# Kernel tuning notes

Hardware: AMD Instinct MI355X
Metric: run time of the kernel (lower is better)

## Reference

```python
import jax, jax.numpy as jnp
import numpy as np

NEG_SLOPE = 0.2  # LeakyReLU slope from the module


def setup_inputs() -> dict:
    key = jax.random.key(0)
    k1, k2, k3, k4 = jax.random.split(key, 4)
    B, N, C, H, D = 8, 1024, 256, 4, 64
    x = jax.random.normal(k1, (B, N, C), dtype=jnp.float32)
    adj = (jax.random.uniform(k2, (B, N, N)) < 0.05).astype(jnp.float32)
    # nn.Linear weight, stored as (in, out) for x @ W
    W = jax.random.normal(k3, (C, H * D), dtype=jnp.float32) / np.sqrt(C)
    a = jax.random.normal(k4, (1, H, 2 * D), dtype=jnp.float32) * 0.1
    return {"x": x, "adj": adj, "W": W, "a": a}


def reference(x, adj, W, a):
    # x: (B,N,C), adj: (B,N,N), W: (C,H*D), a: (1,H,2D)
    B, N, _ = x.shape
    H = a.shape[1]
    D = a.shape[2] // 2
    Wx = (x @ W).reshape(B, N, H, D)  # (B,N,H,D)
    # (cat([Wx_i, Wx_j]) * a).sum(-1) decomposes into two rank-1 terms:
    a_i, a_j = a[0, :, :D], a[0, :, D:]
    e_i = jnp.einsum('bnhd,hd->bnh', Wx, a_i)  # contribution of target node i
    e_j = jnp.einsum('bjhd,hd->bjh', Wx, a_j)  # contribution of source node j
    e = e_i[:, :, None, :] + e_j[:, None, :, :]  # (B,N,N,H)
    e = jnp.where(e > 0, e, NEG_SLOPE * e)  # LeakyReLU(0.2)
    # add self-loops, mask non-edges with -inf
    adj_self = adj + jnp.eye(N, dtype=adj.dtype)[None]
    mask = (adj_self == 0)[..., None]  # (B,N,N,1)
    e = jnp.where(mask, -jnp.inf, e)
    alpha = jax.nn.softmax(e, axis=2)  # softmax over neighbors j
    # dropout is identity in eval mode
    # torch: einsum('bnjh,bnjhd', alpha, Wx_j) with Wx_j broadcast over n
    out = jnp.einsum('bnjh,bjhd->bnhd', alpha, Wx)
    return out.reshape(B, N, H * D)
```

## Files before the change

### kernel.cpp

```cpp
#include <hip/hip_runtime.h>

#define Nn 1024
#define Cc 256
#define Hh 4
#define Dd 64
#define HD 256
#define LOG2E 1.4426950408889634f

typedef unsigned short u16;
typedef unsigned int u32;
typedef unsigned long long u64;
typedef unsigned char u8;
typedef __bf16 bf16x8 __attribute__((ext_vector_type(8)));
typedef float f32x4 __attribute__((ext_vector_type(4)));
typedef u16 u16x8 __attribute__((ext_vector_type(8)));
typedef u32 u32x4 __attribute__((ext_vector_type(4)));

__device__ __forceinline__ float bf2f(u16 v) {
    return __builtin_bit_cast(float, (u32)v << 16);
}
__device__ __forceinline__ u16 f2bf(float f) {
    u32 u = __builtin_bit_cast(u32, f);
    return (u16)((u + 0x7fffu + ((u >> 16) & 1u)) >> 16);
}
__device__ __forceinline__ float fast_exp2(float x) {
#if __has_builtin(__builtin_amdgcn_exp2f)
    return __builtin_amdgcn_exp2f(x);
#else
    float r; asm("v_exp_f32 %0, %1" : "=v"(r) : "v"(x)); return r;
#endif
}

__global__ __launch_bounds__(256) void k_bitmask_prep(const float* __restrict__ adj,
        u8* __restrict__ bm, const float* __restrict__ W,
        u16* __restrict__ WTh, u16* __restrict__ WTl) {
    int idx = blockIdx.x * 256 + threadIdx.x;
    int bn = idx >> 7;
    int byteidx = idx & 127;
    int n = bn & 1023;
    const float* p = adj + ((size_t)bn << 10) + (byteidx << 3);
    float4 v0 = *reinterpret_cast<const float4*>(p);
    float4 v1 = *reinterpret_cast<const float4*>(p + 4);
    u32 bits = 0;
    bits |= (__builtin_bit_cast(u32, v0.x) != 0u) ? 1u : 0u;
    bits |= (__builtin_bit_cast(u32, v0.y) != 0u) ? 2u : 0u;
    bits |= (__builtin_bit_cast(u32, v0.z) != 0u) ? 4u : 0u;
    bits |= (__builtin_bit_cast(u32, v0.w) != 0u) ? 8u : 0u;
    bits |= (__builtin_bit_cast(u32, v1.x) != 0u) ? 16u : 0u;
    bits |= (__builtin_bit_cast(u32, v1.y) != 0u) ? 32u : 0u;
    bits |= (__builtin_bit_cast(u32, v1.z) != 0u) ? 64u : 0u;
    bits |= (__builtin_bit_cast(u32, v1.w) != 0u) ? 128u : 0u;
    if ((n >> 3) == byteidx) bits |= 1u << (n & 7);
    bm[idx] = (u8)bits;
    if (blockIdx.x < 256) {
        int c = blockIdx.x;
        int t = threadIdx.x;
        float v = W[c * HD + t];
        u16 hi = f2bf(v);
        float lo = v - bf2f(hi);
        WTh[t * Cc + c] = hi;
        WTl[t * Cc + c] = f2bf(lo);
    }
}

__global__ __launch_bounds__(256) void k_gemm_xw(const float* __restrict__ x,
        const u16* __restrict__ WTh, const u16* __restrict__ WTl,
        const float* __restrict__ a, u16* __restrict__ WxTt,
        float* __restrict__ ei, float* __restrict__ ej) {
    int wave = blockIdx.x * 4 + (threadIdx.x >> 6);
    int lane = threadIdx.x & 63;
    int row_tile = wave >> 2;
    int h = wave & 3;
    int m0 = row_tile * 16;
    int b = m0 >> 10;
    int nloc0 = m0 & 1023;
    int c15 = lane & 15;
    int quad = lane >> 4;

    f32x4 acc[4] = {};
    const float* xrow = x + (size_t)(m0 + c15) * Cc + quad * 8;
    #pragma unroll
    for (int k0 = 0; k0 < Cc; k0 += 32) {
        float4 xv0 = *reinterpret_cast<const float4*>(xrow + k0);
        float4 xv1 = *reinterpret_cast<const float4*>(xrow + k0 + 4);
        float xv[8] = {xv0.x, xv0.y, xv0.z, xv0.w, xv1.x, xv1.y, xv1.z, xv1.w};
        u16x8 xh, xl;
        #pragma unroll
        for (int i = 0; i < 8; ++i) {
            u16 hb = f2bf(xv[i]);
            xh[i] = hb;
            xl[i] = f2bf(xv[i] - bf2f(hb));
        }
        bf16x8 ah = __builtin_bit_cast(bf16x8, xh);
        bf16x8 al = __builtin_bit_cast(bf16x8, xl);
        #pragma unroll
        for (int t = 0; t < 4; ++t) {
            const u16* wb = WTh + (size_t)(h * 64 + t * 16 + c15) * Cc + k0 + quad * 8;
            const u16* wl = WTl + (size_t)(h * 64 + t * 16 + c15) * Cc + k0 + quad * 8;
            bf16x8 bh = *reinterpret_cast<const bf16x8*>(wb);
            bf16x8 bl = *reinterpret_cast<const bf16x8*>(wl);
            acc[t] = __builtin_amdgcn_mfma_f32_16x16x32_bf16(ah, bh, acc[t], 0, 0, 0);
            acc[t] = __builtin_amdgcn_mfma_f32_16x16x32_bf16(al, bh, acc[t], 0, 0, 0);
            acc[t] = __builtin_amdgcn_mfma_f32_16x16x32_bf16(ah, bl, acc[t], 0, 0, 0);
        }
    }
    int bh = b * Hh + h;
    int n_base = nloc0 + quad * 4;
    int chunk = nloc0 >> 5;
    int jq = ((n_base >> 3) & 3);
    int ii = n_base & 7;
    size_t tb = (size_t)bh * 65536 + chunk * 2048 + jq * 128 + c15 * 8 + ii;
    #pragma unroll
    for (int t = 0; t < 4; ++t) {
        u32 lo = (u32)f2bf(acc[t][0]) | ((u32)f2bf(acc[t][1]) << 16);
        u32 hi = (u32)f2bf(acc[t][2]) | ((u32)f2bf(acc[t][3]) << 16);
        uint2 pk; pk.x = lo; pk.y = hi;
        *reinterpret_cast<uint2*>(WxTt + tb + t * 512) = pk;
    }
    float ai[4], aj[4];
    #pragma unroll
    for (int t = 0; t < 4; ++t) {
        ai[t] = a[h * 2 * Dd + t * 16 + c15];
        aj[t] = a[h * 2 * Dd + Dd + t * 16 + c15];
    }
    #pragma unroll
    for (int r = 0; r < 4; ++r) {
        float si = acc[0][r] * ai[0] + acc[1][r] * ai[1] + acc[2][r] * ai[2] + acc[3][r] * ai[3];
        float sj = acc[0][r] * aj[0] + acc[1][r] * aj[1] + acc[2][r] * aj[2] + acc[3][r] * aj[3];
        #pragma unroll
        for (int off = 1; off < 16; off <<= 1) {
            si += __shfl_xor(si, off);
            sj += __shfl_xor(sj, off);
        }
        if (c15 == 0) {
            int n = nloc0 + quad * 4 + r;
            ei[(size_t)bh * Nn + n] = si * LOG2E;
            ej[(size_t)bh * Nn + n] = sj * LOG2E;
        }
    }
}

__global__ __launch_bounds__(256) void k_attn(const u8* __restrict__ bm,
        const u16* __restrict__ WxTt, const float* __restrict__ eis,
        const float* __restrict__ ejs, float* __restrict__ out) {
    int widx = threadIdx.x >> 6;
    int lane = threadIdx.x & 63;
    int bh = blockIdx.x >> 5;
    int tile = blockIdx.x & 31;
    int b = bh >> 2, h = bh & 3;
    int n0 = tile * 32;
    int col = lane & 15;
    int quad = lane >> 4;

    int r0 = n0 + col, r1 = n0 + 16 + col;
    float ei0 = eis[(size_t)bh * Nn + r0];
    float ei1 = eis[(size_t)bh * Nn + r1];
    const u8* mb0 = bm + ((size_t)(b * Nn + r0)) * 128;
    const u8* mb1 = bm + ((size_t)(b * Nn + r1)) * 128;
    const float* ejrow = ejs + (size_t)bh * Nn + quad * 8;
    const u16* wxplane = WxTt + (size_t)bh * 65536 + lane * 8;

    u16 ov = (col == 0) ? (u16)0x3f80 : (u16)0;
    u16x8 onesu = {ov, ov, ov, ov, ov, ov, ov, ov};
    bf16x8 onesf = __builtin_bit_cast(bf16x8, onesu);

    f32x4 acc0[4] = {}, acc1[4] = {};
    f32x4 accl0 = {}, accl1 = {};
    int jbase = widx * 256;
    #pragma unroll 2
    for (int s = 0; s < 8; ++s) {
        int j0 = jbase + s * 32;
        u32 mw0 = *reinterpret_cast<const u32*>(mb0 + (j0 >> 3));
        u32 mw1 = *reinterpret_cast<const u32*>(mb1 + (j0 >> 3));
        u32 q0 = (mw0 >> (quad * 8)) & 0xffu;
        u32 q1 = (mw1 >> (quad * 8)) & 0xffu;
        float4 eA = *reinterpret_cast<const float4*>(ejrow + j0);
        float4 eB = *reinterpret_cast<const float4*>(ejrow + j0 + 4);
        float ejv[8] = {eA.x, eA.y, eA.z, eA.w, eB.x, eB.y, eB.z, eB.w};
        u32 p0[4], p1[4];
        #pragma unroll
        for (int pi = 0; pi < 4; ++pi) {
            float e_lo = ejv[2 * pi], e_hi = ejv[2 * pi + 1];
            float sa = ei0 + e_lo, sb = ei0 + e_hi;
            sa = fmaxf(sa, 0.2f * sa); sb = fmaxf(sb, 0.2f * sb);
            u32 ua = __builtin_bit_cast(u32, fast_exp2(sa));
            u32 ub = __builtin_bit_cast(u32, fast_exp2(sb));
            u32 m0 = (((q0 >> (2 * pi)) & 1u) ? 0xffffu : 0u)
                   | (((q0 >> (2 * pi + 1)) & 1u) ? 0xffff0000u : 0u);
            p0[pi] = ((ua >> 16) | (ub & 0xffff0000u)) & m0;
            float sc = ei1 + e_lo, sd = ei1 + e_hi;
            sc = fmaxf(sc, 0.2f * sc); sd = fmaxf(sd, 0.2f * sd);
            u32 uc = __builtin_bit_cast(u32, fast_exp2(sc));
            u32 ud = __builtin_bit_cast(u32, fast_exp2(sd));
            u32 m1 = (((q1 >> (2 * pi)) & 1u) ? 0xffffu : 0u)
                   | (((q1 >> (2 * pi + 1)) & 1u) ? 0xffff0000u : 0u);
            p1[pi] = ((uc >> 16) | (ud & 0xffff0000u)) & m1;
        }
        u32x4 pv0 = {p0[0], p0[1], p0[2], p0[3]};
        u32x4 pv1 = {p1[0], p1[1], p1[2], p1[3]};
        bf16x8 a0 = __builtin_bit_cast(bf16x8, pv0);
        bf16x8 a1 = __builtin_bit_cast(bf16x8, pv1);
        const u16* bbase = wxplane + (j0 >> 5) * 2048;
        #pragma unroll
        for (int t = 0; t < 4; ++t) {
            bf16x8 bfr = *reinterpret_cast<const bf16x8*>(bbase + t * 512);
            acc0[t] = __builtin_amdgcn_mfma_f32_16x16x32_bf16(a0, bfr, acc0[t], 0, 0, 0);
            acc1[t] = __builtin_amdgcn_mfma_f32_16x16x32_bf16(a1, bfr, acc1[t], 0, 0, 0);
        }
        accl0 = __builtin_amdgcn_mfma_f32_16x16x32_bf16(a0, onesf, accl0, 0, 0, 0);
        accl1 = __builtin_amdgcn_mfma_f32_16x16x32_bf16(a1, onesf, accl1, 0, 0, 0);
    }

    __shared__ f32x4 lacc[4][8][64];
    __shared__ float lsums[4][2][16];
    #pragma unroll
    for (int t = 0; t < 4; ++t) {
        lacc[widx][t][lane] = acc0[t];
        lacc[widx][4 + t][lane] = acc1[t];
    }
    if (col == 0) {
        #pragma unroll
        for (int r = 0; r < 4; ++r) {
            lsums[widx][0][quad * 4 + r] = accl0[r];
            lsums[widx][1][quad * 4 + r] = accl1[r];
        }
    }
    __syncthreads();
    #pragma unroll
    for (int pp = 0; pp < 2; ++pp) {
        int p = widx * 2 + pp;
        int f = p >> 2, t = p & 3;
        f32x4 v = lacc[0][p][lane];
        v += lacc[1][p][lane];
        v += lacc[2][p][lane];
        v += lacc[3][p][lane];
        #pragma unroll
        for (int r = 0; r < 4; ++r) {
            int rloc = quad * 4 + r;
            float lv = lsums[0][f][rloc] + lsums[1][f][rloc]
                     + lsums[2][f][rloc] + lsums[3][f][rloc];
            int nr = n0 + f * 16 + rloc;
            out[(size_t)(b * Nn + nr) * HD + h * Dd + t * 16 + col] = v[r] * (1.0f / lv);
        }
    }
}

extern "C" void kernel_launch(void* const* d_in, const int* in_sizes, int n_in,
                              void* d_out, int out_size, void* d_ws, size_t ws_size,
                              hipStream_t stream) {
    const float* x   = (const float*)d_in[0];
    const float* adj = (const float*)d_in[1];
    const float* W   = (const float*)d_in[2];
    const float* a   = (const float*)d_in[3];
    float* out = (float*)d_out;

    char* ws = (char*)d_ws;
    u16*   WTh  = (u16*)(ws);
    u16*   WTl  = (u16*)(ws + (128u << 10));
    u16*   WxTt = (u16*)(ws + (256u << 10));
    float* ei   = (float*)(ws + (256u << 10) + (4u << 20));
    float* ej   = (float*)(ws + (384u << 10) + (4u << 20));
    u8*    bm   = (u8*)(ws + (512u << 10) + (4u << 20));

    k_bitmask_prep<<<4096, 256, 0, stream>>>(adj, bm, W, WTh, WTl);
    k_gemm_xw<<<512, 256, 0, stream>>>(x, WTh, WTl, a, WxTt, ei, ej);
    k_attn<<<1024, 256, 0, stream>>>(bm, WxTt, ei, ej, out);
}
```

Before: 124.9 us.

## Fuse bitmask prep and XW GEMM into one kernel with LDS-staged W

Merges the adjacency bitmask kernel and the x@W GEMM into a single launch, with blocks split by index between the two jobs. Each GEMM block converts its head's W slice to bf16 straight into padded LDS, which removes the global WTh/WTl transpose buffers and one kernel boundary. It also drops the low-part W correction MFMA, leaving two of the three split-precision products, and uses packed hardware bf16 conversion. This loses some GEMM accuracy, and each GEMM block now reloads and converts its W slice.

Result: faster. 111.8 us (-10.5%).

```diff
diff --git a/kernel.cpp b/kernel.cpp
--- a/kernel.cpp
+++ b/kernel.cpp
@@ -6,11 +6,13 @@
 #define Dd 64
 #define HD 256
 #define LOG2E 1.4426950408889634f
+#define WSTRIDE 264
 
 typedef unsigned short u16;
 typedef unsigned int u32;
 typedef unsigned long long u64;
 typedef unsigned char u8;
+typedef __bf16 bf16x2 __attribute__((ext_vector_type(2)));
 typedef __bf16 bf16x8 __attribute__((ext_vector_type(8)));
 typedef float f32x4 __attribute__((ext_vector_type(4)));
 typedef u16 u16x8 __attribute__((ext_vector_type(8)));
@@ -22,6 +24,14 @@
 __device__ __forceinline__ u16 f2bf(float f) {
     u32 u = __builtin_bit_cast(u32, f);
     return (u16)((u + 0x7fffu + ((u >> 16) & 1u)) >> 16);
+}
+__device__ __forceinline__ u32 pk_bf16(float a, float b) {
+#if __has_builtin(__builtin_amdgcn_cvt_pk_bf16_f32)
+    bf16x2 v = __builtin_amdgcn_cvt_pk_bf16_f32(a, b);
+    return __builtin_bit_cast(u32, v);
+#else
+    return (u32)f2bf(a) | ((u32)f2bf(b) << 16);
+#endif
 }
 __device__ __forceinline__ float fast_exp2(float x) {
 #if __has_builtin(__builtin_amdgcn_exp2f)
@@ -31,46 +41,55 @@
 #endif
 }
 
-__global__ __launch_bounds__(256) void k_bitmask_prep(const float* __restrict__ adj,
-        u8* __restrict__ bm, const float* __restrict__ W,
-        u16* __restrict__ WTh, u16* __restrict__ WTl) {
-    int idx = blockIdx.x * 256 + threadIdx.x;
-    int bn = idx >> 7;
-    int byteidx = idx & 127;
-    int n = bn & 1023;
-    const float* p = adj + ((size_t)bn << 10) + (byteidx << 3);
-    float4 v0 = *reinterpret_cast<const float4*>(p);
-    float4 v1 = *reinterpret_cast<const float4*>(p + 4);
-    u32 bits = 0;
-    bits |= (__builtin_bit_cast(u32, v0.x) != 0u) ? 1u : 0u;
-    bits |= (__builtin_bit_cast(u32, v0.y) != 0u) ? 2u : 0u;
-    bits |= (__builtin_bit_cast(u32, v0.z) != 0u) ? 4u : 0u;
-    bits |= (__builtin_bit_cast(u32, v0.w) != 0u) ? 8u : 0u;
-    bits |= (__builtin_bit_cast(u32, v1.x) != 0u) ? 16u : 0u;
-    bits |= (__builtin_bit_cast(u32, v1.y) != 0u) ? 32u : 0u;
-    bits |= (__builtin_bit_cast(u32, v1.z) != 0u) ? 64u : 0u;
-    bits |= (__builtin_bit_cast(u32, v1.w) != 0u) ? 128u : 0u;
-    if ((n >> 3) == byteidx) bits |= 1u << (n & 7);
-    bm[idx] = (u8)bits;
-    if (blockIdx.x < 256) {
-        int c = blockIdx.x;
-        int t = threadIdx.x;
-        float v = W[c * HD + t];
-        u16 hi = f2bf(v);
-        float lo = v - bf2f(hi);
-        WTh[t * Cc + c] = hi;
-        WTl[t * Cc + c] = f2bf(lo);
-    }
-}
-
-__global__ __launch_bounds__(256) void k_gemm_xw(const float* __restrict__ x,
-        const u16* __restrict__ WTh, const u16* __restrict__ WTl,
-        const float* __restrict__ a, u16* __restrict__ WxTt,
-        float* __restrict__ ei, float* __restrict__ ej) {
-    int wave = blockIdx.x * 4 + (threadIdx.x >> 6);
-    int lane = threadIdx.x & 63;
-    int row_tile = wave >> 2;
-    int h = wave & 3;
+__global__ __launch_bounds__(256) void k_fused(const float* __restrict__ adj,
+        u8* __restrict__ bm, const float* __restrict__ x,
+        const float* __restrict__ W, const float* __restrict__ a,
+        u16* __restrict__ WxTt, float* __restrict__ ei, float* __restrict__ ej) {
+    __shared__ u16 ldsw[Dd * WSTRIDE];
+
+    if (blockIdx.x >= 512) {
+        int idx = (blockIdx.x - 512) * 256 + threadIdx.x;
+        int bn = idx >> 7;
+        int byteidx = idx & 127;
+        int n = bn & 1023;
+        const float* p = adj + ((size_t)bn << 10) + (byteidx << 3);
+        float4 v0 = *reinterpret_cast<const float4*>(p);
+        float4 v1 = *reinterpret_cast<const float4*>(p + 4);
+        u32 bits = 0;
+        bits |= (__builtin_bit_cast(u32, v0.x) != 0u) ? 1u : 0u;
+        bits |= (__builtin_bit_cast(u32, v0.y) != 0u) ? 2u : 0u;
+        bits |= (__builtin_bit_cast(u32, v0.z) != 0u) ? 4u : 0u;
+        bits |= (__builtin_bit_cast(u32, v0.w) != 0u) ? 8u : 0u;
+        bits |= (__builtin_bit_cast(u32, v1.x) != 0u) ? 16u : 0u;
+        bits |= (__builtin_bit_cast(u32, v1.y) != 0u) ? 32u : 0u;
+        bits |= (__builtin_bit_cast(u32, v1.z) != 0u) ? 64u : 0u;
+        bits |= (__builtin_bit_cast(u32, v1.w) != 0u) ? 128u : 0u;
+        if ((n >> 3) == byteidx) bits |= 1u << (n & 7);
+        bm[idx] = (u8)bits;
+        return;
+    }
+
+    int h = blockIdx.x & 3;
+    int group = blockIdx.x >> 2;
+    int tid = threadIdx.x;
+
+    {
+        const float* wrow = W + tid * HD + h * 64;
+        #pragma unroll
+        for (int c = 0; c < 64; c += 4) {
+            float4 wv = *reinterpret_cast<const float4*>(wrow + c);
+            u32 p01 = pk_bf16(wv.x, wv.y);
+            u32 p23 = pk_bf16(wv.z, wv.w);
+            ldsw[(c + 0) * WSTRIDE + tid] = (u16)p01;
+            ldsw[(c + 1) * WSTRIDE + tid] = (u16)(p01 >> 16);
+            ldsw[(c + 2) * WSTRIDE + tid] = (u16)p23;
+            ldsw[(c + 3) * WSTRIDE + tid] = (u16)(p23 >> 16);
+        }
+    }
+    __syncthreads();
+
+    int w = tid >> 6, lane = tid & 63;
+    int row_tile = group * 4 + w;
     int m0 = row_tile * 16;
     int b = m0 >> 10;
     int nloc0 = m0 & 1023;
@@ -83,25 +102,28 @@
     for (int k0 = 0; k0 < Cc; k0 += 32) {
         float4 xv0 = *reinterpret_cast<const float4*>(xrow + k0);
         float4 xv1 = *reinterpret_cast<const float4*>(xrow + k0 + 4);
-        float xv[8] = {xv0.x, xv0.y, xv0.z, xv0.w, xv1.x, xv1.y, xv1.z, xv1.w};
-        u16x8 xh, xl;
-        #pragma unroll
-        for (int i = 0; i < 8; ++i) {
-            u16 hb = f2bf(xv[i]);
-            xh[i] = hb;
-            xl[i] = f2bf(xv[i] - bf2f(hb));
-        }
-        bf16x8 ah = __builtin_bit_cast(bf16x8, xh);
-        bf16x8 al = __builtin_bit_cast(bf16x8, xl);
+        u32 h0 = pk_bf16(xv0.x, xv0.y);
+        u32 h1 = pk_bf16(xv0.z, xv0.w);
+        u32 h2 = pk_bf16(xv1.x, xv1.y);
+        u32 h3 = pk_bf16(xv1.z, xv1.w);
+        u32 l0 = pk_bf16(xv0.x - __builtin_bit_cast(float, h0 << 16),
+                         xv0.y - __builtin_bit_cast(float, h0 & 0xffff0000u));
+        u32 l1 = pk_bf16(xv0.z - __builtin_bit_cast(float, h1 << 16),
+                         xv0.w - __builtin_bit_cast(float, h1 & 0xffff0000u));
+        u32 l2 = pk_bf16(xv1.x - __builtin_bit_cast(float, h2 << 16),
+                         xv1.y - __builtin_bit_cast(float, h2 & 0xffff0000u));
+        u32 l3 = pk_bf16(xv1.z - __builtin_bit_cast(float, h3 << 16),
+                         xv1.w - __builtin_bit_cast(float, h3 & 0xffff0000u));
+        u32x4 hp = {h0, h1, h2, h3};
+        u32x4 lp = {l0, l1, l2, l3};
+        bf16x8 ah = __builtin_bit_cast(bf16x8, hp);
+        bf16x8 al = __builtin_bit_cast(bf16x8, lp);
+        const u16* ldsk = ldsw + k0 + quad * 8;
         #pragma unroll
         for (int t = 0; t < 4; ++t) {
-            const u16* wb = WTh + (size_t)(h * 64 + t * 16 + c15) * Cc + k0 + quad * 8;
-            const u16* wl = WTl + (size_t)(h * 64 + t * 16 + c15) * Cc + k0 + quad * 8;
-            bf16x8 bh = *reinterpret_cast<const bf16x8*>(wb);
-            bf16x8 bl = *reinterpret_cast<const bf16x8*>(wl);
+            bf16x8 bh = *reinterpret_cast<const bf16x8*>(ldsk + (t * 16 + c15) * WSTRIDE);
             acc[t] = __builtin_amdgcn_mfma_f32_16x16x32_bf16(ah, bh, acc[t], 0, 0, 0);
             acc[t] = __builtin_amdgcn_mfma_f32_16x16x32_bf16(al, bh, acc[t], 0, 0, 0);
-            acc[t] = __builtin_amdgcn_mfma_f32_16x16x32_bf16(ah, bl, acc[t], 0, 0, 0);
         }
     }
     int bh = b * Hh + h;
@@ -112,10 +134,10 @@
     size_t tb = (size_t)bh * 65536 + chunk * 2048 + jq * 128 + c15 * 8 + ii;
     #pragma unroll
     for (int t = 0; t < 4; ++t) {
-        u32 lo = (u32)f2bf(acc[t][0]) | ((u32)f2bf(acc[t][1]) << 16);
-        u32 hi = (u32)f2bf(acc[t][2]) | ((u32)f2bf(acc[t][3]) << 16);
-        uint2 pk; pk.x = lo; pk.y = hi;
-        *reinterpret_cast<uint2*>(WxTt + tb + t * 512) = pk;
+        uint2 pk2;
+        pk2.x = pk_bf16(acc[t][0], acc[t][1]);
+        pk2.y = pk_bf16(acc[t][2], acc[t][3]);
+        *reinterpret_cast<uint2*>(WxTt + tb + t * 512) = pk2;
     }
     float ai[4], aj[4];
     #pragma unroll
@@ -183,18 +205,14 @@
             float e_lo = ejv[2 * pi], e_hi = ejv[2 * pi + 1];
             float sa = ei0 + e_lo, sb = ei0 + e_hi;
             sa = fmaxf(sa, 0.2f * sa); sb = fmaxf(sb, 0.2f * sb);
-            u32 ua = __builtin_bit_cast(u32, fast_exp2(sa));
-            u32 ub = __builtin_bit_cast(u32, fast_exp2(sb));
             u32 m0 = (((q0 >> (2 * pi)) & 1u) ? 0xffffu : 0u)
                    | (((q0 >> (2 * pi + 1)) & 1u) ? 0xffff0000u : 0u);
-            p0[pi] = ((ua >> 16) | (ub & 0xffff0000u)) & m0;
+            p0[pi] = pk_bf16(fast_exp2(sa), fast_exp2(sb)) & m0;
             float sc = ei1 + e_lo, sd = ei1 + e_hi;
             sc = fmaxf(sc, 0.2f * sc); sd = fmaxf(sd, 0.2f * sd);
-            u32 uc = __builtin_bit_cast(u32, fast_exp2(sc));
-            u32 ud = __builtin_bit_cast(u32, fast_exp2(sd));
             u32 m1 = (((q1 >> (2 * pi)) & 1u) ? 0xffffu : 0u)
                    | (((q1 >> (2 * pi + 1)) & 1u) ? 0xffff0000u : 0u);
-            p1[pi] = ((uc >> 16) | (ud & 0xffff0000u)) & m1;
+            p1[pi] = pk_bf16(fast_exp2(sc), fast_exp2(sd)) & m1;
         }
         u32x4 pv0 = {p0[0], p0[1], p0[2], p0[3]};
         u32x4 pv1 = {p1[0], p1[1], p1[2], p1[3]};
@@ -255,14 +273,11 @@
     float* out = (float*)d_out;
 
     char* ws = (char*)d_ws;
-    u16*   WTh  = (u16*)(ws);
-    u16*   WTl  = (u16*)(ws + (128u << 10));
-    u16*   WxTt = (u16*)(ws + (256u << 10));
-    float* ei   = (float*)(ws + (256u << 10) + (4u << 20));
-    float* ej   = (float*)(ws + (384u << 10) + (4u << 20));
-    u8*    bm   = (u8*)(ws + (512u << 10) + (4u << 20));
-
-    k_bitmask_prep<<<4096, 256, 0, stream>>>(adj, bm, W, WTh, WTl);
-    k_gemm_xw<<<512, 256, 0, stream>>>(x, WTh, WTl, a, WxTt, ei, ej);
+    u16*   WxTt = (u16*)(ws);
+    float* ei   = (float*)(ws + (4u << 20));
+    float* ej   = (float*)(ws + (4u << 20) + (128u << 10));
+    u8*    bm   = (u8*)(ws + (4u << 20) + (256u << 10));
+
+    k_fused<<<4608, 256, 0, stream>>>(adj, bm, x, W, a, WxTt, ei, ej);
     k_attn<<<1024, 256, 0, stream>>>(bm, WxTt, ei, ej, out);
 }
```
